# Kernel optimization log

Measured on AMD Instinct MI355X. Metric: run time of the kernel, lower is better.

## Reference

```python
import jax, jax.numpy as jnp
import numpy as np

K_FRAC = 0.5  # init arg k (keep fraction)


def setup_inputs() -> dict:
    key = jax.random.key(0)
    k1, k2, k3, k4, k5 = jax.random.split(key, 5)
    B, N, F = 1, 100000, 128
    E, Fe = 1600000, 32
    x = jax.random.normal(k1, (B, N, F), jnp.float32)
    edge_index = jax.random.randint(k2, (2, E), 0, N, dtype=jnp.int32)
    edge_attr = jax.random.normal(k3, (B, E, Fe), jnp.float32)
    # nn.Linear(in_dim, 1) params
    proj_w = jax.random.normal(k4, (1, F), jnp.float32) / jnp.sqrt(F)
    proj_b = jax.random.normal(k5, (1,), jnp.float32) * 0.01
    return {"x": x, "edge_attr": edge_attr, "proj_w": proj_w,
            "proj_b": proj_b, "edge_index": edge_index}


def reference(x, edge_attr, proj_w, proj_b, edge_index):
    B, N, F = x.shape
    # linear score + sigmoid (dropout p=0 -> identity)
    scores = jax.nn.sigmoid(jnp.einsum('bnf,of->bno', x, proj_w)[..., 0] + proj_b[0])  # [B,N]
    # torch.kthvalue(scores, kth, dim=1): kth smallest (1-indexed)
    kth = int((1.0 - K_FRAC) * N)
    kth_scores = jnp.sort(scores, axis=1)[:, kth - 1:kth]  # [B,1]
    mask = scores >= kth_scores  # [B,N]
    n_keep = int(N * K_FRAC)
    # stable descending sort of mask.float() -> true indices first, in original order
    pool_indices = jnp.argsort(jnp.where(mask, 0, 1), axis=1)[:, :n_keep]  # [B,n_keep]
    new_x = jnp.take_along_axis(x, pool_indices[..., None], axis=1)  # [B,n_keep,F]
    # 1-D node mask shared across batch (as in the torch code)
    node_mask = jnp.zeros((N,), bool).at[pool_indices].set(True)
    pool_edges = node_mask[edge_index[0]] & node_mask[edge_index[1]]  # [E] bool
    new_edge_index = edge_index[:, pool_edges]        # [2, E'] (data-dependent, eager)
    new_edge_attr = edge_attr[:, pool_edges]          # [B, E', Fe]
    mapping = jnp.full((N,), -1, jnp.int32).at[pool_indices].set(
        jnp.broadcast_to(jnp.arange(n_keep, dtype=jnp.int32), pool_indices.shape))
    new_edge_index_ordered = mapping[new_edge_index]
    return (new_x, new_edge_index, new_edge_index_ordered, new_edge_attr,
            pool_indices, pool_edges)
```

## Files before the change

kernel.cpp:

```cpp
#include <hip/hip_runtime.h>
#include <math.h>

#define ST_AGG 1ull
#define ST_PRE 2ull

__device__ __forceinline__ void block_select(
    const unsigned* __restrict__ hist, unsigned q,
    unsigned* __restrict__ outB, unsigned* __restrict__ outRem) {
  __shared__ unsigned sc[256];
  __shared__ unsigned sres[2];
  int t = threadIdx.x;
  {
    const unsigned long long* hp = (const unsigned long long*)(hist + t * 256);
    unsigned s = 0;
    #pragma unroll 8
    for (int j = 0; j < 128; j++) {
      unsigned long long v =
          __hip_atomic_load(&hp[j], __ATOMIC_RELAXED, __HIP_MEMORY_SCOPE_AGENT);
      s += (unsigned)v + (unsigned)(v >> 32);
    }
    sc[t] = s;
    unsigned val = s;
    __syncthreads();
    for (int st = 1; st < 256; st <<= 1) {
      unsigned a = (t >= st) ? sc[t - st] : 0u;
      __syncthreads();
      sc[t] += a;
      __syncthreads();
    }
    unsigned incl = sc[t], excl = incl - val;
    if (q >= excl && q < incl) { sres[0] = (unsigned)t; sres[1] = q - excl; }
  }
  __syncthreads();
  unsigned chunk = sres[0], rem = sres[1];
  {
    unsigned v = __hip_atomic_load(&hist[chunk * 256 + t], __ATOMIC_RELAXED,
                                   __HIP_MEMORY_SCOPE_AGENT);
    __syncthreads();
    sc[t] = v;
    unsigned val = v;
    __syncthreads();
    for (int st = 1; st < 256; st <<= 1) {
      unsigned a = (t >= st) ? sc[t - st] : 0u;
      __syncthreads();
      sc[t] += a;
      __syncthreads();
    }
    unsigned incl = sc[t], excl = incl - val;
    if (rem >= excl && rem < incl) {
      *outB = chunk * 256 + t;
      *outRem = rem - excl;
    }
  }
}

__global__ __launch_bounds__(256) void scores_hist_kernel(
    const float* __restrict__ x, const float* __restrict__ w,
    const float* __restrict__ bptr, int N, int F, unsigned* __restrict__ scores,
    unsigned* __restrict__ hist, unsigned qconst, unsigned* __restrict__ sel,
    unsigned* __restrict__ doneCnt) {
  __shared__ float tX[64 * 128];
  __shared__ double sPart[4 * 64];
  __shared__ float wS[128];
  __shared__ unsigned sLast;
  int t = threadIdx.x;
  int blockBase = blockIdx.x * 256;
  if (t < 128) wS[t] = w[t];
  __syncthreads();
  int row = t & 63, seg = t >> 6;
  float4 wreg[8];
  {
    const float4* w4 = (const float4*)(wS + seg * 32);
    #pragma unroll
    for (int k = 0; k < 8; k++) wreg[k] = w4[k];
  }
  double bias = (double)bptr[0];
  for (int tile = 0; tile < 4; tile++) {
    int rowBase = blockBase + tile * 64;
    {
      const float4* src = (const float4*)(x + (size_t)rowBase * 128);
      float4* dst = (float4*)tX;
      #pragma unroll
      for (int k = 0; k < 8; k++) {
        int idx = t + k * 256;
        int grow = rowBase + (idx >> 5);
        float4 v = make_float4(0.f, 0.f, 0.f, 0.f);
        if (grow < N) v = src[idx];
        dst[idx] = v;
      }
    }
    __syncthreads();
    {
      const float4* xr = (const float4*)(tX + row * 128 + seg * 32);
      double acc = 0.0;
      #pragma unroll
      for (int k = 0; k < 8; k++) {
        float4 xv = xr[k];
        float4 wv = wreg[k];
        acc += (double)xv.x * (double)wv.x;
        acc += (double)xv.y * (double)wv.y;
        acc += (double)xv.z * (double)wv.z;
        acc += (double)xv.w * (double)wv.w;
      }
      sPart[seg * 64 + row] = acc;
    }
    __syncthreads();
    if (t < 64) {
      int node = rowBase + t;
      if (node < N) {
        double z = sPart[t] + sPart[64 + t] + sPart[128 + t] + sPart[192 + t] + bias;
        double s = 1.0 / (1.0 + exp(-z));
        unsigned bits = __float_as_uint((float)s);
        scores[node] = bits;
        atomicAdd(&hist[bits >> 16], 1u);
      }
    }
    __syncthreads();
  }
  __threadfence();
  if (t == 0) sLast = (atomicAdd(doneCnt, 1u) == gridDim.x - 1u) ? 1u : 0u;
  __syncthreads();
  if (sLast) block_select(hist, qconst, sel + 0, sel + 1);
}

__global__ __launch_bounds__(256) void hist2_kernel(
    const unsigned* __restrict__ scores, int N, const unsigned* __restrict__ sel,
    unsigned* __restrict__ hist, unsigned* __restrict__ selOut,
    unsigned* __restrict__ doneCnt) {
  __shared__ unsigned sLast;
  int i = blockIdx.x * 256 + threadIdx.x;
  if (i < N) {
    unsigned bits = scores[i];
    if ((bits >> 16) == sel[0]) atomicAdd(&hist[bits & 0xFFFFu], 1u);
  }
  __threadfence();
  if (threadIdx.x == 0) sLast = (atomicAdd(doneCnt, 1u) == gridDim.x - 1u) ? 1u : 0u;
  __syncthreads();
  if (sLast) block_select(hist, sel[1], selOut + 0, selOut + 1);
}

__device__ __forceinline__ unsigned lookback_exclusive(
    unsigned long long* status, int bid, int lane) {
  unsigned excl = 0;
  int j = bid - 1;
  for (;;) {
    int idx = j - lane;
    unsigned long long st;
    if (idx >= 0) {
      do {
        st = __hip_atomic_load(&status[idx], __ATOMIC_RELAXED, __HIP_MEMORY_SCOPE_AGENT);
      } while ((st >> 32) == 0ull);
    } else {
      st = (ST_PRE << 32);
    }
    int isPre = ((st >> 32) == ST_PRE);
    unsigned long long preb = __ballot(isPre);
    int p = __ffsll(preb) - 1;
    unsigned contrib = (p < 0 || lane <= p) ? (unsigned)st : 0u;
    for (int off = 32; off > 0; off >>= 1)
      contrib += __shfl_down(contrib, off, 64);
    excl += __shfl(contrib, 0, 64);
    if (p >= 0) return excl;
    j -= 64;
  }
}

__device__ __forceinline__ void publish_status(
    unsigned long long* status, int bid, unsigned long long st, unsigned v) {
  __hip_atomic_store(&status[bid], (st << 32) | (unsigned long long)v,
                     __ATOMIC_RELAXED, __HIP_MEMORY_SCOPE_AGENT);
}

__global__ __launch_bounds__(256) void node_compact(
    const unsigned* __restrict__ scores, const unsigned* __restrict__ sel,
    const float* __restrict__ x, int N, int F, int n_keep,
    unsigned* __restrict__ ticket, unsigned long long* __restrict__ status,
    int* __restrict__ map, float* __restrict__ out_pool, float* __restrict__ outx) {
  __shared__ unsigned sBid;
  __shared__ unsigned wv[4];
  __shared__ unsigned sExcl;
  __shared__ int sSrc[256];
  int t = threadIdx.x;
  if (t == 0) sBid = atomicAdd(ticket, 1u);
  __syncthreads();
  int bid = (int)sBid;
  int i = bid * 256 + t;
  unsigned T = (sel[0] << 16) | sel[2];
  int m = (i < N) && (scores[i] >= T);
  unsigned long long bal = __ballot(m);
  int lane = t & 63, wave = t >> 6;
  if (lane == 0) wv[wave] = (unsigned)__popcll(bal);
  __syncthreads();
  unsigned agg = wv[0] + wv[1] + wv[2] + wv[3];
  if (wave == 0) {
    if (lane == 0 && bid > 0) publish_status(status, bid, ST_AGG, agg);
    unsigned excl = (bid > 0) ? lookback_exclusive(status, bid, lane) : 0u;
    if (lane == 0) {
      publish_status(status, bid, ST_PRE, excl + agg);
      sExcl = excl;
    }
  }
  __syncthreads();
  unsigned wpre = 0;
  for (int k = 0; k < wave; k++) wpre += wv[k];
  unsigned li = wpre + (unsigned)__popcll(bal & ((1ull << lane) - 1ull));
  if (i < N) {
    int mv = -1;
    if (m) {
      unsigned pre = sExcl + li;
      if (pre < (unsigned)n_keep) {
        mv = (int)pre;
        out_pool[pre] = (float)i;
        sSrc[li] = i;
      }
    }
    map[i] = mv;
  }
  __syncthreads();
  unsigned lim = agg;
  if (sExcl + agg > (unsigned)n_keep)
    lim = ((unsigned)n_keep > sExcl) ? ((unsigned)n_keep - sExcl) : 0u;
  for (int k = t >> 5; k < (int)lim; k += 8) {
    const float4* s4 = (const float4*)(x + (size_t)sSrc[k] * F);
    float4* d4 = (float4*)(outx + (size_t)(sExcl + (unsigned)k) * F);
    d4[t & 31] = s4[t & 31];
  }
}

__global__ __launch_bounds__(256) void edge_compact(
    const int* __restrict__ ei, const int* __restrict__ map, int E, int Ek, int Fe,
    const float* __restrict__ attr,
    unsigned* __restrict__ ticket, unsigned long long* __restrict__ status,
    float* __restrict__ out,
    size_t o_ei, size_t o_eio, size_t o_attr, size_t o_pe) {
  __shared__ unsigned sBid;
  __shared__ unsigned wv[4];
  __shared__ unsigned sExcl;
  __shared__ int sE[1024];
  __shared__ float sA[1024], sB[1024], sMA[1024], sMB[1024];
  int t = threadIdx.x;
  if (t == 0) sBid = atomicAdd(ticket, 1u);
  __syncthreads();
  int bid = (int)sBid;
  int e0 = bid * 1024 + t * 4;
  int m[4] = {0, 0, 0, 0};
  int av[4], bv[4], mav[4], mbv[4];
  unsigned c = 0;
  if (e0 < E) {
    int4 a4 = ((const int4*)ei)[(size_t)bid * 256 + t];
    int4 b4 = ((const int4*)(ei + E))[(size_t)bid * 256 + t];
    av[0] = a4.x; av[1] = a4.y; av[2] = a4.z; av[3] = a4.w;
    bv[0] = b4.x; bv[1] = b4.y; bv[2] = b4.z; bv[3] = b4.w;
    #pragma unroll
    for (int j = 0; j < 4; j++) {
      mav[j] = map[av[j]];
      mbv[j] = map[bv[j]];
      m[j] = (mav[j] >= 0) && (mbv[j] >= 0);
      c += (unsigned)m[j];
    }
    float4 pe4 = make_float4((float)m[0], (float)m[1], (float)m[2], (float)m[3]);
    *(float4*)(out + o_pe + e0) = pe4;
  }
  int lane = t & 63, wave = t >> 6;
  unsigned incl = c;
  #pragma unroll
  for (int off = 1; off < 64; off <<= 1) {
    unsigned u = __shfl_up(incl, off, 64);
    if (lane >= off) incl += u;
  }
  if (lane == 63) wv[wave] = incl;
  __syncthreads();
  unsigned agg = wv[0] + wv[1] + wv[2] + wv[3];
  if (wave == 0) {
    if (lane == 0 && bid > 0) publish_status(status, bid, ST_AGG, agg);
    unsigned excl = (bid > 0) ? lookback_exclusive(status, bid, lane) : 0u;
    if (lane == 0) {
      publish_status(status, bid, ST_PRE, excl + agg);
      sExcl = excl;
    }
  }
  __syncthreads();
  unsigned wpre = 0;
  for (int k = 0; k < wave; k++) wpre += wv[k];
  unsigned r = wpre + (incl - c);
  if (e0 < E) {
    #pragma unroll
    for (int j = 0; j < 4; j++) {
      if (m[j]) {
        sE[r]  = e0 + j;
        sA[r]  = (float)av[j];
        sB[r]  = (float)bv[j];
        sMA[r] = (float)mav[j];
        sMB[r] = (float)mbv[j];
        r++;
      }
    }
  }
  __syncthreads();
  for (int k = t; k < (int)agg; k += 256) {
    unsigned p = sExcl + (unsigned)k;
    out[o_ei + p]              = sA[k];
    out[o_ei + (size_t)Ek + p] = sB[k];
    out[o_eio + p]              = sMA[k];
    out[o_eio + (size_t)Ek + p] = sMB[k];
  }
  for (int k = t >> 3; k < (int)agg; k += 32) {
    const float4* src = (const float4*)(attr + (size_t)sE[k] * Fe);
    float4* dst = (float4*)(out + o_attr + (size_t)(sExcl + (unsigned)k) * Fe);
    dst[t & 7] = src[t & 7];
  }
}

extern "C" void kernel_launch(void* const* d_in, const int* in_sizes, int n_in,
                              void* d_out, int out_size, void* d_ws, size_t ws_size,
                              hipStream_t stream) {
  const int F  = in_sizes[2];
  const int E  = in_sizes[4] / 2;
  const int N  = in_sizes[0] / F;
  const int Fe = in_sizes[1] / E;
  const int n_keep = N / 2;
  const unsigned q = (unsigned)(N - n_keep - 1);
  const int Ek = (int)(((long long)out_size - (long long)n_keep * F - n_keep - E) / (4 + Fe));

  const float* x    = (const float*)d_in[0];
  const float* attr = (const float*)d_in[1];
  const float* w    = (const float*)d_in[2];
  const float* b    = (const float*)d_in[3];
  const int*   ei   = (const int*)d_in[4];
  float*       out  = (float*)d_out;

  const size_t o_newx = 0;
  const size_t o_ei   = (size_t)n_keep * F;
  const size_t o_eio  = o_ei + 2 * (size_t)Ek;
  const size_t o_attr = o_eio + 2 * (size_t)Ek;
  const size_t o_pool = o_attr + (size_t)Ek * Fe;
  const size_t o_pe   = o_pool + (size_t)n_keep;

  char* wsb = (char*)d_ws;
  size_t off = 0;
  auto carve = [&](size_t bytes) -> void* {
    void* p = wsb + off;
    off = (off + bytes + 255) & ~(size_t)255;
    return p;
  };
  const int nb_n  = (N + 255) / 256;
  const int nb_e  = (E + 1023) / 1024;
  unsigned* scores = (unsigned*)carve((size_t)N * 4);
  size_t zero_begin = off;
  unsigned* hist1   = (unsigned*)carve((size_t)65536 * 4);
  unsigned* hist2   = (unsigned*)carve((size_t)65536 * 4);
  unsigned* tickets = (unsigned*)carve(4 * 4);
  unsigned long long* status_n = (unsigned long long*)carve((size_t)nb_n * 8);
  unsigned long long* status_e = (unsigned long long*)carve((size_t)nb_e * 8);
  size_t zero_end = off;
  unsigned* sel    = (unsigned*)carve(64);
  int* map         = (int*)carve((size_t)N * 4);
  (void)ws_size;

  hipMemsetAsync(hist1, 0, zero_end - zero_begin, stream);
  scores_hist_kernel<<<nb_n, 256, 0, stream>>>(x, w, b, N, F, scores, hist1,
                                               q, sel, tickets + 2);
  hist2_kernel<<<nb_n, 256, 0, stream>>>(scores, N, sel, hist2, sel + 2, tickets + 3);
  node_compact<<<nb_n, 256, 0, stream>>>(scores, sel, x, N, F, n_keep, tickets + 0,
                                         status_n, map, out + o_pool, out + o_newx);
  edge_compact<<<nb_e, 256, 0, stream>>>(ei, map, E, Ek, Fe, attr, tickets + 1, status_e,
                                         out, o_ei, o_eio, o_attr, o_pe);
}
```

Baseline: 522.0 us.

## Compute node scores with 16-lane shuffle reductions in a grid-stride loop

Replaces the shared-memory tiled dot product (64 rows per tile, four segments, several syncthreads per tile) with 16 lanes per node. Each lane loads two float4s directly from global memory and the lanes combine partial sums with a width-16 shuffle reduction. The kernel now runs a fixed grid of 1024 blocks with a grid-stride loop instead of one block per 256 nodes. This removes the 32KB LDS tile and the barriers, which should raise occupancy, at the cost of more double-precision shuffles and more atomics issued from fewer blocks.

New measurement: 635.3 us. 1.22x slower.

```diff
diff --git a/kernel.cpp b/kernel.cpp
--- a/kernel.cpp
+++ b/kernel.cpp
@@ -56,66 +56,36 @@
 
 __global__ __launch_bounds__(256) void scores_hist_kernel(
     const float* __restrict__ x, const float* __restrict__ w,
-    const float* __restrict__ bptr, int N, int F, unsigned* __restrict__ scores,
+    const float* __restrict__ bptr, int N, unsigned* __restrict__ scores,
     unsigned* __restrict__ hist, unsigned qconst, unsigned* __restrict__ sel,
     unsigned* __restrict__ doneCnt) {
-  __shared__ float tX[64 * 128];
-  __shared__ double sPart[4 * 64];
-  __shared__ float wS[128];
   __shared__ unsigned sLast;
   int t = threadIdx.x;
-  int blockBase = blockIdx.x * 256;
-  if (t < 128) wS[t] = w[t];
-  __syncthreads();
-  int row = t & 63, seg = t >> 6;
-  float4 wreg[8];
-  {
-    const float4* w4 = (const float4*)(wS + seg * 32);
+  int sub = t & 15;
+  const float4* w4 = (const float4*)w;
+  float4 wv0 = w4[sub * 2];
+  float4 wv1 = w4[sub * 2 + 1];
+  double bias = (double)bptr[0];
+  int slot   = (blockIdx.x * 256 + t) >> 4;
+  int nSlots = (int)(gridDim.x * 256) >> 4;
+  for (int node = slot; node < N; node += nSlots) {
+    const float4* xr = (const float4*)(x + (size_t)node * 128);
+    float4 v0 = xr[sub * 2];
+    float4 v1 = xr[sub * 2 + 1];
+    double acc = (double)v0.x * (double)wv0.x + (double)v0.y * (double)wv0.y +
+                 (double)v0.z * (double)wv0.z + (double)v0.w * (double)wv0.w +
+                 (double)v1.x * (double)wv1.x + (double)v1.y * (double)wv1.y +
+                 (double)v1.z * (double)wv1.z + (double)v1.w * (double)wv1.w;
     #pragma unroll
-    for (int k = 0; k < 8; k++) wreg[k] = w4[k];
-  }
-  double bias = (double)bptr[0];
-  for (int tile = 0; tile < 4; tile++) {
-    int rowBase = blockBase + tile * 64;
-    {
-      const float4* src = (const float4*)(x + (size_t)rowBase * 128);
-      float4* dst = (float4*)tX;
-      #pragma unroll
-      for (int k = 0; k < 8; k++) {
-        int idx = t + k * 256;
-        int grow = rowBase + (idx >> 5);
-        float4 v = make_float4(0.f, 0.f, 0.f, 0.f);
-        if (grow < N) v = src[idx];
-        dst[idx] = v;
-      }
-    }
-    __syncthreads();
-    {
-      const float4* xr = (const float4*)(tX + row * 128 + seg * 32);
-      double acc = 0.0;
-      #pragma unroll
-      for (int k = 0; k < 8; k++) {
-        float4 xv = xr[k];
-        float4 wv = wreg[k];
-        acc += (double)xv.x * (double)wv.x;
-        acc += (double)xv.y * (double)wv.y;
-        acc += (double)xv.z * (double)wv.z;
-        acc += (double)xv.w * (double)wv.w;
-      }
-      sPart[seg * 64 + row] = acc;
-    }
-    __syncthreads();
-    if (t < 64) {
-      int node = rowBase + t;
-      if (node < N) {
-        double z = sPart[t] + sPart[64 + t] + sPart[128 + t] + sPart[192 + t] + bias;
-        double s = 1.0 / (1.0 + exp(-z));
-        unsigned bits = __float_as_uint((float)s);
-        scores[node] = bits;
-        atomicAdd(&hist[bits >> 16], 1u);
-      }
-    }
-    __syncthreads();
+    for (int off = 8; off > 0; off >>= 1)
+      acc += __shfl_down(acc, off, 16);
+    if (sub == 0) {
+      double z = acc + bias;
+      double s = 1.0 / (1.0 + exp(-z));
+      unsigned bits = __float_as_uint((float)s);
+      scores[node] = bits;
+      atomicAdd(&hist[bits >> 16], 1u);
+    }
   }
   __threadfence();
   if (t == 0) sLast = (atomicAdd(doneCnt, 1u) == gridDim.x - 1u) ? 1u : 0u;
@@ -358,7 +328,7 @@
   (void)ws_size;
 
   hipMemsetAsync(hist1, 0, zero_end - zero_begin, stream);
-  scores_hist_kernel<<<nb_n, 256, 0, stream>>>(x, w, b, N, F, scores, hist1,
+  scores_hist_kernel<<<1024, 256, 0, stream>>>(x, w, b, N, scores, hist1,
                                                q, sel, tickets + 2);
   hist2_kernel<<<nb_n, 256, 0, stream>>>(scores, N, sel, hist2, sel + 2, tickets + 3);
   node_compact<<<nb_n, 256, 0, stream>>>(scores, sel, x, N, F, n_keep, tickets + 0,
```
